# Kernel optimization log

Measured on AMD Instinct MI355X. Metric: run time of the kernel, lower is better.

The kernel has to match this reference:

```python
import jax, jax.numpy as jnp
import numpy as np

N = 100000      # nodes
E = 3200000     # edges
F = 128         # input features
H = 16          # hiddenSize (hard-coded in source)
C = 10          # num_classes
RATIO = 0.25
K1 = int(np.ceil(RATIO * N))   # 25000 nodes kept by pool1
K2 = int(np.ceil(RATIO * K1))  # 6250 nodes kept by pool2


def gcn_conv(x, W, b, src, dst, ew, n):
    """PyG GCNConv: add self-loops (weight 1), symmetric normalization.
    ew carries edge validity mask / weights; ew=0 edges are exactly equivalent
    to removed edges (contribute nothing to degree or aggregation)."""
    h = x @ W                                                   # [n, out]
    deg = jax.ops.segment_sum(ew, dst, num_segments=n) + 1.0    # +1 self-loop
    dinv = jax.lax.rsqrt(deg)
    norm = dinv[src] * dinv[dst] * ew                           # [E]
    agg = jax.ops.segment_sum(h[src] * norm[:, None], dst, num_segments=n)
    agg = agg + h * (dinv * dinv)[:, None]                      # self-loop msg
    return agg + b


def graph_conv_score(x, wroot, wrel, b, src, dst, ew, n):
    """PyG GraphConv (SAGPooling default GNN) with out_channels=1:
    score_i = x_i @ Wroot + (sum_j x_j) @ Wrel + b."""
    agg = jax.ops.segment_sum(x[src] * ew[:, None], dst, num_segments=n)
    return (x @ wroot + agg @ wrel + b).reshape(-1)             # [n]


def sag_pool(x, src, dst, ew, wroot, wrel, b, n, k):
    """SAGPooling: score -> top-k -> x[perm]*tanh(score[perm]) -> filter_adj.
    filter_adj is expressed by relabeling kept nodes and zeroing dropped edges
    (math-identical to edge removal for downstream GCN/GraphConv)."""
    score = graph_conv_score(x, wroot, wrel, b, src, dst, ew, n)
    vals, perm = jax.lax.top_k(score, k)
    xp = x[perm] * jnp.tanh(vals)[:, None]
    new_idx = jnp.full((n,), -1, dtype=jnp.int32).at[perm].set(
        jnp.arange(k, dtype=jnp.int32))
    ns, nd = new_idx[src], new_idx[dst]
    valid = (ns >= 0) & (nd >= 0)
    new_ew = jnp.where(valid, ew, 0.0)
    ns = jnp.where(valid, ns, 0)
    nd = jnp.where(valid, nd, 0)
    return xp, ns, nd, new_ew


def setup_inputs() -> dict:
    key = jax.random.key(0)
    ks = jax.random.split(key, 9)
    s = 0.1
    return {
        "x": jax.random.normal(ks[0], (N, F), jnp.float32),
        "edge_src": jax.random.randint(ks[1], (E,), 0, N, dtype=jnp.int32),
        "edge_dst": jax.random.randint(ks[2], (E,), 0, N, dtype=jnp.int32),
        "W1": jax.random.normal(ks[3], (F, H), jnp.float32) * s,
        "b1": jnp.zeros((H,), jnp.float32),
        "p1_wroot": jax.random.normal(ks[4], (H, 1), jnp.float32) * s,
        "p1_wrel": jax.random.normal(ks[5], (H, 1), jnp.float32) * s,
        "p1_b": jnp.zeros((1,), jnp.float32),
        "W2": jax.random.normal(ks[6], (H, C), jnp.float32) * s,
        "b2": jnp.zeros((C,), jnp.float32),
        "p2_wroot": jax.random.normal(ks[7], (C, 1), jnp.float32) * s,
        "p2_wrel": jax.random.normal(ks[8], (C, 1), jnp.float32) * s,
        "p2_b": jnp.zeros((1,), jnp.float32),
    }


def reference(x, edge_src, edge_dst, W1, b1, p1_wroot, p1_wrel, p1_b,
              W2, b2, p2_wroot, p2_wrel, p2_b):
    ew0 = jnp.ones((E,), x.dtype)
    # conv1 + relu (dropout is identity in eval mode)
    h = jax.nn.relu(gcn_conv(x, W1, b1, edge_src, edge_dst, ew0, N))
    # pool1 (ratio 0.25)
    x1, s1, d1, ew1 = sag_pool(h, edge_src, edge_dst, ew0,
                               p1_wroot, p1_wrel, p1_b, N, K1)
    # conv2
    h2 = gcn_conv(x1, W2, b2, s1, d1, ew1, K1)
    # pool2 (ratio 0.25)
    x2, s2, d2, ew2 = sag_pool(h2, s1, d1, ew1,
                               p2_wroot, p2_wrel, p2_b, K1, K2)
    # global mean pool over the single graph, then log_softmax
    out = jnp.mean(x2, axis=0, keepdims=True)   # [1, C]
    return jax.nn.log_softmax(out, axis=1)
```

## Files before the change

### kernel.cpp

```cpp
#include <hip/hip_runtime.h>
#include <math.h>

#define NN 100000
#define EE 3200000
#define FF 128
#define HH 16
#define CC 10
#define PC 12
#define KK1 25000
#define KK2 6250

#define NBIN 512
#define BUCK_SHIFT 8
#define BUCK_MASK 255
#define ABLK 256
#define EPB (EE / ABLK)
#define NBUCK ((NN + 255) / 256)

struct SelState {
  unsigned prefix;
  unsigned kcur;
  unsigned ctr_gt;
  unsigned ctr_eq;
  unsigned hist[256];
};

__device__ __forceinline__ unsigned fkey(float f) {
  unsigned u = __float_as_uint(f);
  return (u & 0x80000000u) ? ~u : (u | 0x80000000u);
}

__global__ __launch_bounds__(256) void k_xw1(const float* __restrict__ x,
                                             const float* __restrict__ W1,
                                             float* __restrict__ h0) {
  __shared__ float sW[FF * HH];
  __shared__ float sx[16][FF];
  int t = threadIdx.x;
  for (int i = t; i < FF * HH; i += 256) sW[i] = W1[i];
  int base = blockIdx.x * 16;
  for (int i = t; i < 16 * FF; i += 256) {
    int r = i >> 7, c = i & 127;
    int node = base + r;
    sx[r][c] = (node < NN) ? x[(size_t)node * FF + c] : 0.f;
  }
  __syncthreads();
  int r = t >> 4;
  int o = t & 15;
  float acc = 0.f;
#pragma unroll
  for (int k = 0; k < FF; ++k) acc += sx[r][k] * sW[k * HH + o];
  int node = base + r;
  if (node < NN) h0[node * HH + o] = acc;
}

__global__ __launch_bounds__(256) void k_bhist(const int* __restrict__ dst,
                                               unsigned* __restrict__ Hist) {
  __shared__ unsigned sh[NBIN];
  int t = threadIdx.x;
  for (int i = t; i < NBIN; i += 256) sh[i] = 0;
  __syncthreads();
  int base = blockIdx.x * EPB;
  for (int i = base + t; i < base + EPB; i += 256)
    atomicAdd(&sh[dst[i] >> BUCK_SHIFT], 1u);
  __syncthreads();
  for (int i = t; i < NBIN; i += 256) Hist[blockIdx.x * NBIN + i] = sh[i];
}

__global__ __launch_bounds__(64) void k_bcursor(unsigned* __restrict__ Hist,
                                                unsigned* __restrict__ Tot) {
  int bin = blockIdx.x * 64 + threadIdx.x;
  unsigned run = 0;
#pragma unroll 8
  for (int b = 0; b < ABLK; ++b) {
    unsigned c = Hist[b * NBIN + bin];
    Hist[b * NBIN + bin] = run;
    run += c;
  }
  Tot[bin] = run;
}

__global__ __launch_bounds__(512) void k_bscan(const unsigned* __restrict__ Tot,
                                               unsigned* __restrict__ BucketOff) {
  __shared__ unsigned s[NBIN];
  int t = threadIdx.x;
  unsigned v = Tot[t];
  s[t] = v;
  __syncthreads();
  for (int off = 1; off < NBIN; off <<= 1) {
    unsigned u = (t >= off) ? s[t - off] : 0;
    __syncthreads();
    s[t] += u;
    __syncthreads();
  }
  BucketOff[t] = s[t] - v;
  if (t == NBIN - 1) BucketOff[NBIN] = s[t];
}

__global__ __launch_bounds__(256) void k_bscatter(const int* __restrict__ src,
                                                  const int* __restrict__ dst,
                                                  const unsigned* __restrict__ Hist,
                                                  const unsigned* __restrict__ BucketOff,
                                                  unsigned* __restrict__ packed) {
  __shared__ unsigned cur[NBIN];
  int t = threadIdx.x;
  for (int i = t; i < NBIN; i += 256)
    cur[i] = BucketOff[i] + Hist[blockIdx.x * NBIN + i];
  __syncthreads();
  int base = blockIdx.x * EPB;
  for (int i = base + t; i < base + EPB; i += 256) {
    int d = dst[i];
    unsigned pos = atomicAdd(&cur[d >> BUCK_SHIFT], 1u);
    packed[pos] = ((unsigned)(d & BUCK_MASK) << 17) | (unsigned)src[i];
  }
}

__global__ __launch_bounds__(256) void k_bfine(const unsigned* __restrict__ packed,
                                               const unsigned* __restrict__ BucketOff,
                                               int* __restrict__ rowstart,
                                               float* __restrict__ dinv,
                                               int* __restrict__ csr) {
  __shared__ unsigned fcnt[256], fpos[256], fcur[256];
  int bin = blockIdx.x;
  int t = threadIdx.x;
  unsigned b0 = BucketOff[bin], b1 = BucketOff[bin + 1];
  fcnt[t] = 0;
  __syncthreads();
  for (unsigned e = b0 + t; e < b1; e += 256)
    atomicAdd(&fcnt[packed[e] >> 17], 1u);
  __syncthreads();
  unsigned v = fcnt[t];
  fpos[t] = v;
  __syncthreads();
  for (int off = 1; off < 256; off <<= 1) {
    unsigned u = (t >= off) ? fpos[t - off] : 0;
    __syncthreads();
    fpos[t] += u;
    __syncthreads();
  }
  unsigned excl = fpos[t] - v;
  fcur[t] = b0 + excl;
  int node = bin * 256 + t;
  if (node < NN) {
    rowstart[node] = (int)(b0 + excl);
    dinv[node] = rsqrtf((float)v + 1.0f);
  }
  if (bin == 0 && t == 0) rowstart[NN] = EE;
  __syncthreads();
  for (unsigned e = b0 + t; e < b1; e += 256) {
    unsigned p = packed[e];
    unsigned pos = atomicAdd(&fcur[p >> 17], 1u);
    csr[pos] = (int)(p & 0x1FFFFu);
  }
}

__global__ __launch_bounds__(256) void k_conv1(const float* __restrict__ h0,
                                               const float* __restrict__ dinv,
                                               const int* __restrict__ rowstart,
                                               const int* __restrict__ csr,
                                               const float* __restrict__ b1,
                                               const float* __restrict__ wroot,
                                               const float* __restrict__ wrel,
                                               const float* __restrict__ bp,
                                               float* __restrict__ h,
                                               float* __restrict__ score,
                                               float* __restrict__ hrel) {
  int node = blockIdx.x * 4 + (threadIdx.x >> 6);
  if (node >= NN) return;
  int lane = threadIdx.x & 63;
  int eslot = lane >> 2;
  int kq = lane & 3;
  int s0 = rowstart[node], s1 = rowstart[node + 1];
  float ax = 0.f, ay = 0.f, az = 0.f, aw = 0.f;
  for (int base = s0; base < s1; base += 16) {
    int idx = base + eslot;
    bool on = idx < s1;
    int sv = on ? csr[idx] : 0;
    float dv = on ? dinv[sv] : 0.f;
    float4 hv = *(const float4*)(h0 + sv * HH + kq * 4);
    ax += hv.x * dv;
    ay += hv.y * dv;
    az += hv.z * dv;
    aw += hv.w * dv;
  }
#pragma unroll
  for (int m = 4; m <= 32; m <<= 1) {
    ax += __shfl_xor(ax, m);
    ay += __shfl_xor(ay, m);
    az += __shfl_xor(az, m);
    aw += __shfl_xor(aw, m);
  }
  float di = dinv[node];
  float4 hs = *(const float4*)(h0 + node * HH + kq * 4);
  float vx = ax * di + hs.x * di * di + b1[kq * 4 + 0];
  float vy = ay * di + hs.y * di * di + b1[kq * 4 + 1];
  float vz = az * di + hs.z * di * di + b1[kq * 4 + 2];
  float vw = aw * di + hs.w * di * di + b1[kq * 4 + 3];
  vx = vx > 0.f ? vx : 0.f;
  vy = vy > 0.f ? vy : 0.f;
  vz = vz > 0.f ? vz : 0.f;
  vw = vw > 0.f ? vw : 0.f;
  if (eslot == 0) {
    float4 o4 = make_float4(vx, vy, vz, vw);
    *(float4*)(h + node * HH + kq * 4) = o4;
  }
  float sr = vx * wroot[kq * 4] + vy * wroot[kq * 4 + 1] +
             vz * wroot[kq * 4 + 2] + vw * wroot[kq * 4 + 3];
  float sl = vx * wrel[kq * 4] + vy * wrel[kq * 4 + 1] +
             vz * wrel[kq * 4 + 2] + vw * wrel[kq * 4 + 3];
  sr += __shfl_xor(sr, 1);
  sr += __shfl_xor(sr, 2);
  sl += __shfl_xor(sl, 1);
  sl += __shfl_xor(sl, 2);
  if (lane == 0) {
    score[node] = sr + bp[0];
    hrel[node] = sl;
  }
}

__global__ __launch_bounds__(256) void k_scoreg(const int* __restrict__ rowstart,
                                                const int* __restrict__ csr,
                                                const float* __restrict__ hrel,
                                                float* __restrict__ score) {
  int node = blockIdx.x * 16 + (threadIdx.x >> 4);
  if (node >= NN) return;
  int lane = threadIdx.x & 15;
  int s0 = rowstart[node], s1 = rowstart[node + 1];
  float sum = 0.f;
  for (int e = s0 + lane; e < s1; e += 16) sum += hrel[csr[e]];
#pragma unroll
  for (int m = 8; m; m >>= 1) sum += __shfl_xor(sum, m, 16);
  if (lane == 0) score[node] += sum;
}

__global__ void k_state_init(SelState* st, int K) {
  if (threadIdx.x == 0) {
    st->prefix = 0;
    st->kcur = (unsigned)K;
    st->ctr_gt = 0;
    st->ctr_eq = 0;
  }
  st->hist[threadIdx.x] = 0;
}

__global__ __launch_bounds__(256) void k_hist(const float* __restrict__ vals, int n,
                                              SelState* st, int pass) {
  __shared__ unsigned sh[256];
  int t = threadIdx.x;
  sh[t] = 0;
  __syncthreads();
  int i = blockIdx.x * 256 + t;
  if (i < n) {
    unsigned key = fkey(vals[i]);
    bool ok = true;
    if (pass != 0) ok = (key >> (32 - 8 * pass)) == st->prefix;
    if (ok) atomicAdd(&sh[(key >> (24 - 8 * pass)) & 255], 1u);
  }
  __syncthreads();
  if (sh[t]) atomicAdd(&st->hist[t], sh[t]);
}

__global__ __launch_bounds__(256) void k_scan(SelState* st) {
  __shared__ unsigned s[256];
  int t = threadIdx.x;
  unsigned kcur = st->kcur;
  unsigned v = st->hist[t];
  s[t] = v;
  __syncthreads();
  for (int off = 1; off < 256; off <<= 1) {
    unsigned u = (t + off < 256) ? s[t + off] : 0;
    __syncthreads();
    s[t] += u;
    __syncthreads();
  }
  unsigned Sme = s[t];
  unsigned Snext = (t < 255) ? s[t + 1] : 0;
  if (Sme >= kcur && Snext < kcur) {
    st->prefix = (st->prefix << 8) | (unsigned)t;
    st->kcur = kcur - Snext;
  }
  st->hist[t] = 0;
}

__global__ void k_select1(const float* __restrict__ score, const float* __restrict__ h,
                          SelState* st, int* __restrict__ new_idx,
                          int* __restrict__ orig_of, float* __restrict__ x1) {
  int i = blockIdx.x * blockDim.x + threadIdx.x;
  if (i >= NN) return;
  float sc = score[i];
  unsigned key = fkey(sc);
  unsigned T = st->prefix;
  int id = -1;
  if (key > T) {
    id = (int)atomicAdd(&st->ctr_gt, 1u);
  } else if (key == T) {
    unsigned p = atomicAdd(&st->ctr_eq, 1u);
    unsigned kneed = st->kcur;
    if (p < kneed) id = (KK1 - (int)kneed) + (int)p;
  }
  new_idx[i] = id;
  if (id >= 0) {
    orig_of[id] = i;
    float tv = tanhf(sc);
#pragma unroll
    for (int k = 0; k < HH; ++k) x1[id * HH + k] = h[i * HH + k] * tv;
  }
}

__global__ __launch_bounds__(256) void k_deg2(const int* __restrict__ orig_of,
                                              const int* __restrict__ rowstart,
                                              const int* __restrict__ csr,
                                              const int* __restrict__ nidx,
                                              float* __restrict__ dinv2) {
  int j = blockIdx.x * 16 + (threadIdx.x >> 4);
  if (j >= KK1) return;
  int lane = threadIdx.x & 15;
  int o = orig_of[j];
  int s0 = rowstart[o], s1 = rowstart[o + 1];
  int c = 0;
  for (int e = s0 + lane; e < s1; e += 16) c += (nidx[csr[e]] >= 0) ? 1 : 0;
#pragma unroll
  for (int m = 8; m; m >>= 1) c += __shfl_xor(c, m, 16);
  if (lane == 0) dinv2[j] = rsqrtf((float)c + 1.0f);
}

__global__ void k_xw2(const float* __restrict__ x1, const float* __restrict__ W2,
                      float* __restrict__ h20) {
  int t = blockIdx.x * blockDim.x + threadIdx.x;
  if (t >= KK1 * PC) return;
  int node = t / PC;
  int o = t - node * PC;
  float acc = 0.f;
  if (o < CC) {
#pragma unroll
    for (int k = 0; k < HH; ++k) acc += x1[node * HH + k] * W2[k * CC + o];
  }
  h20[t] = acc;
}

__global__ __launch_bounds__(256) void k_conv2(const float* __restrict__ h20,
                                               const float* __restrict__ dinv2,
                                               const int* __restrict__ orig_of,
                                               const int* __restrict__ rowstart,
                                               const int* __restrict__ csr,
                                               const int* __restrict__ nidx,
                                               const float* __restrict__ b2,
                                               const float* __restrict__ wroot,
                                               const float* __restrict__ wrel,
                                               const float* __restrict__ bp,
                                               float* __restrict__ h2,
                                               float* __restrict__ score2,
                                               float* __restrict__ h2rel) {
  int j = blockIdx.x * 4 + (threadIdx.x >> 6);
  if (j >= KK1) return;
  int lane = threadIdx.x & 63;
  int eslot = lane >> 2;
  int kq = lane & 3;
  int o = orig_of[j];
  int s0 = rowstart[o], s1 = rowstart[o + 1];
  float ax = 0.f, ay = 0.f, az = 0.f, aw = 0.f;
  for (int base = s0; base < s1; base += 16) {
    int idx = base + eslot;
    bool on = idx < s1;
    int sv = on ? nidx[csr[idx]] : -1;
    float dv = (sv >= 0) ? dinv2[sv] : 0.f;
    int sva = (sv >= 0) ? sv : 0;
    float4 hv = *(const float4*)(h20 + sva * PC + ((kq < 3) ? kq * 4 : 8));
    if (kq == 3) dv = 0.f;
    ax += hv.x * dv;
    ay += hv.y * dv;
    az += hv.z * dv;
    aw += hv.w * dv;
  }
#pragma unroll
  for (int m = 4; m <= 32; m <<= 1) {
    ax += __shfl_xor(ax, m);
    ay += __shfl_xor(ay, m);
    az += __shfl_xor(az, m);
    aw += __shfl_xor(aw, m);
  }
  float di = dinv2[j];
  int kb = (kq < 3) ? kq * 4 : 8;
  float4 hs = *(const float4*)(h20 + j * PC + kb);
  float bx = (kb + 0 < CC) ? b2[kb + 0] : 0.f;
  float by = (kb + 1 < CC) ? b2[kb + 1] : 0.f;
  float bz = (kb + 2 < CC) ? b2[kb + 2] : 0.f;
  float bw = (kb + 3 < CC) ? b2[kb + 3] : 0.f;
  float vx = ax * di + hs.x * di * di + bx;
  float vy = ay * di + hs.y * di * di + by;
  float vz = az * di + hs.z * di * di + bz;
  float vw = aw * di + hs.w * di * di + bw;
  if (kq == 3) { vx = vy = vz = vw = 0.f; }
  if (kb + 2 >= CC) vz = 0.f;
  if (kb + 3 >= CC) vw = 0.f;
  if (eslot == 0 && kq < 3) {
    float4 o4 = make_float4(vx, vy, vz, vw);
    *(float4*)(h2 + j * PC + kq * 4) = o4;
  }
  float wrx = (kb + 0 < CC) ? wroot[kb + 0] : 0.f;
  float wry = (kb + 1 < CC) ? wroot[kb + 1] : 0.f;
  float wrz = (kb + 2 < CC) ? wroot[kb + 2] : 0.f;
  float wrw = (kb + 3 < CC) ? wroot[kb + 3] : 0.f;
  float wlx = (kb + 0 < CC) ? wrel[kb + 0] : 0.f;
  float wly = (kb + 1 < CC) ? wrel[kb + 1] : 0.f;
  float wlz = (kb + 2 < CC) ? wrel[kb + 2] : 0.f;
  float wlw = (kb + 3 < CC) ? wrel[kb + 3] : 0.f;
  float sr = (kq == 3) ? 0.f : (vx * wrx + vy * wry + vz * wrz + vw * wrw);
  float sl = (kq == 3) ? 0.f : (vx * wlx + vy * wly + vz * wlz + vw * wlw);
  sr += __shfl_xor(sr, 1);
  sr += __shfl_xor(sr, 2);
  sl += __shfl_xor(sl, 1);
  sl += __shfl_xor(sl, 2);
  if (lane == 0) {
    score2[j] = sr + bp[0];
    h2rel[j] = sl;
  }
}

__global__ __launch_bounds__(256) void k_score2g(const int* __restrict__ orig_of,
                                                 const int* __restrict__ rowstart,
                                                 const int* __restrict__ csr,
                                                 const int* __restrict__ nidx,
                                                 const float* __restrict__ h2rel,
                                                 float* __restrict__ score2) {
  int j = blockIdx.x * 16 + (threadIdx.x >> 4);
  if (j >= KK1) return;
  int lane = threadIdx.x & 15;
  int o = orig_of[j];
  int s0 = rowstart[o], s1 = rowstart[o + 1];
  float sum = 0.f;
  for (int e = s0 + lane; e < s1; e += 16) {
    int s = nidx[csr[e]];
    if (s >= 0) sum += h2rel[s];
  }
#pragma unroll
  for (int m = 8; m; m >>= 1) sum += __shfl_xor(sum, m, 16);
  if (lane == 0) score2[j] += sum;
}

__global__ __launch_bounds__(256) void k_final_accum(const float* __restrict__ score,
                                                     const float* __restrict__ h2,
                                                     SelState* st, float* __restrict__ acc) {
  int i = blockIdx.x * blockDim.x + threadIdx.x;
  float tv = 0.f;
  if (i < KK1) {
    float sc = score[i];
    unsigned key = fkey(sc);
    unsigned T = st->prefix;
    bool keep = false;
    if (key > T) {
      keep = true;
    } else if (key == T) {
      unsigned p = atomicAdd(&st->ctr_eq, 1u);
      keep = (p < st->kcur);
    }
    if (keep) tv = tanhf(sc);
  }
  __shared__ float sacc[CC];
  if (threadIdx.x < CC) sacc[threadIdx.x] = 0.f;
  __syncthreads();
#pragma unroll
  for (int c = 0; c < CC; ++c) {
    float v = (i < KK1 && tv != 0.f) ? h2[i * PC + c] * tv : 0.f;
#pragma unroll
    for (int m = 32; m; m >>= 1) v += __shfl_xor(v, m, 64);
    if ((threadIdx.x & 63) == 0) atomicAdd(&sacc[c], v);
  }
  __syncthreads();
  if (threadIdx.x < CC) atomicAdd(&acc[threadIdx.x], sacc[threadIdx.x]);
}

__global__ void k_final(const float* __restrict__ acc, float* __restrict__ out) {
  if (threadIdx.x != 0 || blockIdx.x != 0) return;
  float v[CC];
  float m = -1e30f;
#pragma unroll
  for (int c = 0; c < CC; ++c) {
    v[c] = acc[c] / (float)KK2;
    if (v[c] > m) m = v[c];
  }
  float s = 0.f;
#pragma unroll
  for (int c = 0; c < CC; ++c) s += expf(v[c] - m);
  float l = logf(s);
#pragma unroll
  for (int c = 0; c < CC; ++c) out[c] = v[c] - m - l;
}

extern "C" void kernel_launch(void* const* d_in, const int* in_sizes, int n_in,
                              void* d_out, int out_size, void* d_ws, size_t ws_size,
                              hipStream_t stream) {
  const float* x      = (const float*)d_in[0];
  const int*   esrc   = (const int*)d_in[1];
  const int*   edst   = (const int*)d_in[2];
  const float* W1     = (const float*)d_in[3];
  const float* b1     = (const float*)d_in[4];
  const float* w1root = (const float*)d_in[5];
  const float* w1rel  = (const float*)d_in[6];
  const float* p1b    = (const float*)d_in[7];
  const float* W2     = (const float*)d_in[8];
  const float* b2     = (const float*)d_in[9];
  const float* w2root = (const float*)d_in[10];
  const float* w2rel  = (const float*)d_in[11];
  const float* p2b    = (const float*)d_in[12];
  float* out = (float*)d_out;

  char* w = (char*)d_ws;
  size_t off = 0;
  auto alloc = [&](size_t bytes) -> char* {
    char* p = w + off;
    off += (bytes + 255) & ~(size_t)255;
    return p;
  };
  float*    h0      = (float*)alloc((size_t)NN * HH * 4);
  float*    hbuf    = (float*)alloc((size_t)NN * HH * 4);
  float*    dinv1   = (float*)alloc((size_t)NN * 4);
  float*    hrel1   = (float*)alloc((size_t)NN * 4);
  float*    score1  = (float*)alloc((size_t)NN * 4);
  int*      nidx    = (int*)  alloc((size_t)NN * 4);
  int*      csr     = (int*)  alloc((size_t)EE * 4);
  unsigned* packed  = (unsigned*)alloc((size_t)EE * 4);
  int*      rowst   = (int*)  alloc((size_t)(NN + 1) * 4);
  unsigned* Hist    = (unsigned*)alloc((size_t)ABLK * NBIN * 4);
  unsigned* Tot     = (unsigned*)alloc((size_t)NBIN * 4);
  unsigned* BOff    = (unsigned*)alloc((size_t)(NBIN + 1) * 4);
  SelState* st1     = (SelState*)alloc(sizeof(SelState));
  SelState* st2     = (SelState*)alloc(sizeof(SelState));
  float*    acc     = (float*)alloc(256);

  size_t off2 = 0;
  auto alloc2 = [&](size_t bytes) -> char* {
    char* p = (char*)h0 + off2;
    off2 += (bytes + 255) & ~(size_t)255;
    return p;
  };
  float* x1      = (float*)alloc2((size_t)KK1 * HH * 4);
  float* h20     = (float*)alloc2((size_t)KK1 * PC * 4 + 256);
  float* h2      = (float*)alloc2((size_t)KK1 * PC * 4 + 256);
  float* dinv2   = (float*)alloc2((size_t)KK1 * 4);
  float* h2rel   = (float*)alloc2((size_t)KK1 * 4);
  float* score2  = (float*)alloc2((size_t)KK1 * 4);
  int*   orig_of = (int*)  alloc2((size_t)KK1 * 4);

  const int BN  = (NN + 255) / 256;
  const int BK1 = (KK1 + 255) / 256;

  k_xw1<<<NN / 16, 256, 0, stream>>>(x, W1, h0);

  k_bhist<<<ABLK, 256, 0, stream>>>(edst, Hist);
  k_bcursor<<<NBIN / 64, 64, 0, stream>>>(Hist, Tot);
  k_bscan<<<1, NBIN, 0, stream>>>(Tot, BOff);
  k_bscatter<<<ABLK, 256, 0, stream>>>(esrc, edst, Hist, BOff, packed);
  k_bfine<<<NBUCK, 256, 0, stream>>>(packed, BOff, rowst, dinv1, csr);

  k_conv1<<<(NN + 3) / 4, 256, 0, stream>>>(h0, dinv1, rowst, csr, b1, w1root, w1rel,
                                            p1b, hbuf, score1, hrel1);
  k_scoreg<<<(NN + 15) / 16, 256, 0, stream>>>(rowst, csr, hrel1, score1);

  k_state_init<<<1, 256, 0, stream>>>(st1, KK1);
  for (int p = 0; p < 4; ++p) {
    k_hist<<<BN, 256, 0, stream>>>(score1, NN, st1, p);
    k_scan<<<1, 256, 0, stream>>>(st1);
  }
  k_select1<<<BN, 256, 0, stream>>>(score1, hbuf, st1, nidx, orig_of, x1);

  k_deg2<<<(KK1 + 15) / 16, 256, 0, stream>>>(orig_of, rowst, csr, nidx, dinv2);
  k_xw2<<<(KK1 * PC + 255) / 256, 256, 0, stream>>>(x1, W2, h20);
  k_conv2<<<(KK1 + 3) / 4, 256, 0, stream>>>(h20, dinv2, orig_of, rowst, csr, nidx,
                                             b2, w2root, w2rel, p2b, h2, score2, h2rel);
  k_score2g<<<(KK1 + 15) / 16, 256, 0, stream>>>(orig_of, rowst, csr, nidx, h2rel, score2);

  k_state_init<<<1, 256, 0, stream>>>(st2, KK2);
  for (int p = 0; p < 4; ++p) {
    k_hist<<<BK1, 256, 0, stream>>>(score2, KK1, st2, p);
    k_scan<<<1, 256, 0, stream>>>(st2);
  }
  hipMemsetAsync(acc, 0, CC * 4, stream);
  k_final_accum<<<BK1, 256, 0, stream>>>(score2, h2, st2, acc);
  k_final<<<1, 64, 0, stream>>>(acc, out);
}
```

Baseline: 477.9 us.

## Merge small kernels, unroll conv1 gather, and use ballot-based compaction in select

Several independent kernels are merged into combined launches: the two state inits and the acc memset become one kernel, xw1 and the bucket histogram share a grid, bcursor and bscan become one block, and deg2 and xw2 share a grid. The conv1 edge loop is unrolled four ways with separate accumulators to expose more memory-level parallelism. The select kernel replaces per-thread global atomics with wave ballots and one atomic per block. The goal is fewer launches and less atomic contention. The single-block bcursor_scan serializes 256 row reads per thread, which may be slower than the old 8-block version.

```diff
diff --git a/kernel.cpp b/kernel.cpp
--- a/kernel.cpp
+++ b/kernel.cpp
@@ -16,6 +16,10 @@
 #define ABLK 256
 #define EPB (EE / ABLK)
 #define NBUCK ((NN + 255) / 256)
+#define XW1_BLKS (NN / 16)
+
+#define DEG2_BLKS ((KK1 + 15) / 16)
+#define XW2_BLKS ((KK1 * PC + 255) / 256)
 
 struct SelState {
   unsigned prefix;
@@ -30,60 +34,66 @@
   return (u & 0x80000000u) ? ~u : (u | 0x80000000u);
 }
 
-__global__ __launch_bounds__(256) void k_xw1(const float* __restrict__ x,
-                                             const float* __restrict__ W1,
-                                             float* __restrict__ h0) {
-  __shared__ float sW[FF * HH];
-  __shared__ float sx[16][FF];
+__global__ __launch_bounds__(512) void k_state_combo(SelState* st1, SelState* st2,
+                                                     float* acc) {
   int t = threadIdx.x;
-  for (int i = t; i < FF * HH; i += 256) sW[i] = W1[i];
-  int base = blockIdx.x * 16;
-  for (int i = t; i < 16 * FF; i += 256) {
-    int r = i >> 7, c = i & 127;
-    int node = base + r;
-    sx[r][c] = (node < NN) ? x[(size_t)node * FF + c] : 0.f;
-  }
-  __syncthreads();
-  int r = t >> 4;
-  int o = t & 15;
-  float acc = 0.f;
-#pragma unroll
-  for (int k = 0; k < FF; ++k) acc += sx[r][k] * sW[k * HH + o];
-  int node = base + r;
-  if (node < NN) h0[node * HH + o] = acc;
-}
-
-__global__ __launch_bounds__(256) void k_bhist(const int* __restrict__ dst,
-                                               unsigned* __restrict__ Hist) {
-  __shared__ unsigned sh[NBIN];
+  unsigned* a1 = (unsigned*)st1;
+  unsigned* a2 = (unsigned*)st2;
+  const int W = sizeof(SelState) / 4;
+  if (t < W) a1[t] = 0u;
+  if (t < W) a2[t] = 0u;
+  if (t < CC) acc[t] = 0.f;
+  if (t == 0) { st1->kcur = KK1; st2->kcur = KK2; }
+}
+
+__global__ __launch_bounds__(256) void k_xw1_bhist(const float* __restrict__ x,
+                                                   const float* __restrict__ W1,
+                                                   float* __restrict__ h0,
+                                                   const int* __restrict__ dst,
+                                                   unsigned* __restrict__ Hist) {
+  __shared__ float smem[FF * HH + 16 * FF];
+  int b = blockIdx.x;
   int t = threadIdx.x;
-  for (int i = t; i < NBIN; i += 256) sh[i] = 0;
-  __syncthreads();
-  int base = blockIdx.x * EPB;
-  for (int i = base + t; i < base + EPB; i += 256)
-    atomicAdd(&sh[dst[i] >> BUCK_SHIFT], 1u);
-  __syncthreads();
-  for (int i = t; i < NBIN; i += 256) Hist[blockIdx.x * NBIN + i] = sh[i];
-}
-
-__global__ __launch_bounds__(64) void k_bcursor(unsigned* __restrict__ Hist,
-                                                unsigned* __restrict__ Tot) {
-  int bin = blockIdx.x * 64 + threadIdx.x;
-  unsigned run = 0;
-#pragma unroll 8
-  for (int b = 0; b < ABLK; ++b) {
-    unsigned c = Hist[b * NBIN + bin];
-    Hist[b * NBIN + bin] = run;
-    run += c;
-  }
-  Tot[bin] = run;
-}
-
-__global__ __launch_bounds__(512) void k_bscan(const unsigned* __restrict__ Tot,
-                                               unsigned* __restrict__ BucketOff) {
+  if (b < XW1_BLKS) {
+    float* sW = smem;
+    float* sx = smem + FF * HH;
+    for (int i = t; i < FF * HH; i += 256) sW[i] = W1[i];
+    int base = b * 16;
+    for (int i = t; i < 16 * FF; i += 256) {
+      int r = i >> 7, c = i & 127;
+      sx[r * FF + c] = x[(size_t)(base + r) * FF + c];
+    }
+    __syncthreads();
+    int r = t >> 4;
+    int o = t & 15;
+    float acc = 0.f;
+#pragma unroll
+    for (int k = 0; k < FF; ++k) acc += sx[r * FF + k] * sW[k * HH + o];
+    h0[(base + r) * HH + o] = acc;
+  } else {
+    unsigned* sh = (unsigned*)smem;
+    int blk = b - XW1_BLKS;
+    for (int i = t; i < NBIN; i += 256) sh[i] = 0;
+    __syncthreads();
+    int base = blk * EPB;
+    for (int i = base + t; i < base + EPB; i += 256)
+      atomicAdd(&sh[dst[i] >> BUCK_SHIFT], 1u);
+    __syncthreads();
+    for (int i = t; i < NBIN; i += 256) Hist[blk * NBIN + i] = sh[i];
+  }
+}
+
+__global__ __launch_bounds__(512) void k_bcursor_scan(unsigned* __restrict__ Hist,
+                                                      unsigned* __restrict__ BucketOff) {
   __shared__ unsigned s[NBIN];
   int t = threadIdx.x;
-  unsigned v = Tot[t];
+  unsigned run = 0;
+  for (int b = 0; b < ABLK; ++b) {
+    unsigned c = Hist[b * NBIN + t];
+    Hist[b * NBIN + t] = run;
+    run += c;
+  }
+  unsigned v = run;
   s[t] = v;
   __syncthreads();
   for (int off = 1; off < NBIN; off <<= 1) {
@@ -170,18 +180,35 @@
   int eslot = lane >> 2;
   int kq = lane & 3;
   int s0 = rowstart[node], s1 = rowstart[node + 1];
-  float ax = 0.f, ay = 0.f, az = 0.f, aw = 0.f;
-  for (int base = s0; base < s1; base += 16) {
-    int idx = base + eslot;
-    bool on = idx < s1;
-    int sv = on ? csr[idx] : 0;
-    float dv = on ? dinv[sv] : 0.f;
-    float4 hv = *(const float4*)(h0 + sv * HH + kq * 4);
-    ax += hv.x * dv;
-    ay += hv.y * dv;
-    az += hv.z * dv;
-    aw += hv.w * dv;
-  }
+  float4 a0 = make_float4(0.f, 0.f, 0.f, 0.f);
+  float4 a1 = a0, a2 = a0, a3 = a0;
+  for (int base = s0; base < s1; base += 64) {
+    int i0 = base + eslot;
+    int i1 = base + 16 + eslot;
+    int i2 = base + 32 + eslot;
+    int i3 = base + 48 + eslot;
+    bool o0 = i0 < s1, o1 = i1 < s1, o2 = i2 < s1, o3 = i3 < s1;
+    int v0 = o0 ? csr[i0] : 0;
+    int v1 = o1 ? csr[i1] : 0;
+    int v2 = o2 ? csr[i2] : 0;
+    int v3 = o3 ? csr[i3] : 0;
+    float d0 = o0 ? dinv[v0] : 0.f;
+    float d1 = o1 ? dinv[v1] : 0.f;
+    float d2 = o2 ? dinv[v2] : 0.f;
+    float d3 = o3 ? dinv[v3] : 0.f;
+    float4 h0v = *(const float4*)(h0 + v0 * HH + kq * 4);
+    float4 h1v = *(const float4*)(h0 + v1 * HH + kq * 4);
+    float4 h2v = *(const float4*)(h0 + v2 * HH + kq * 4);
+    float4 h3v = *(const float4*)(h0 + v3 * HH + kq * 4);
+    a0.x += h0v.x * d0; a0.y += h0v.y * d0; a0.z += h0v.z * d0; a0.w += h0v.w * d0;
+    a1.x += h1v.x * d1; a1.y += h1v.y * d1; a1.z += h1v.z * d1; a1.w += h1v.w * d1;
+    a2.x += h2v.x * d2; a2.y += h2v.y * d2; a2.z += h2v.z * d2; a2.w += h2v.w * d2;
+    a3.x += h3v.x * d3; a3.y += h3v.y * d3; a3.z += h3v.z * d3; a3.w += h3v.w * d3;
+  }
+  float ax = (a0.x + a1.x) + (a2.x + a3.x);
+  float ay = (a0.y + a1.y) + (a2.y + a3.y);
+  float az = (a0.z + a1.z) + (a2.z + a3.z);
+  float aw = (a0.w + a1.w) + (a2.w + a3.w);
 #pragma unroll
   for (int m = 4; m <= 32; m <<= 1) {
     ax += __shfl_xor(ax, m);
@@ -232,16 +259,6 @@
   if (lane == 0) score[node] += sum;
 }
 
-__global__ void k_state_init(SelState* st, int K) {
-  if (threadIdx.x == 0) {
-    st->prefix = 0;
-    st->kcur = (unsigned)K;
-    st->ctr_gt = 0;
-    st->ctr_eq = 0;
-  }
-  st->hist[threadIdx.x] = 0;
-}
-
 __global__ __launch_bounds__(256) void k_hist(const float* __restrict__ vals, int n,
                                               SelState* st, int pass) {
   __shared__ unsigned sh[256];
@@ -281,19 +298,49 @@
   st->hist[t] = 0;
 }
 
-__global__ void k_select1(const float* __restrict__ score, const float* __restrict__ h,
-                          SelState* st, int* __restrict__ new_idx,
-                          int* __restrict__ orig_of, float* __restrict__ x1) {
-  int i = blockIdx.x * blockDim.x + threadIdx.x;
+__global__ __launch_bounds__(256) void k_select1(const float* __restrict__ score,
+                                                 const float* __restrict__ h,
+                                                 SelState* st, int* __restrict__ new_idx,
+                                                 int* __restrict__ orig_of,
+                                                 float* __restrict__ x1) {
+  int i = blockIdx.x * 256 + threadIdx.x;
+  int lane = threadIdx.x & 63;
+  int wid = threadIdx.x >> 6;
+  float sc = 0.f;
+  bool gt = false, eq = false;
+  unsigned T = st->prefix;
+  if (i < NN) {
+    sc = score[i];
+    unsigned key = fkey(sc);
+    gt = key > T;
+    eq = key == T;
+  }
+  unsigned long long mgt = __ballot(gt);
+  unsigned long long meq = __ballot(eq);
+  __shared__ int wgt[4], weq[4];
+  if (lane == 0) {
+    wgt[wid] = __popcll(mgt);
+    weq[wid] = __popcll(meq);
+  }
+  __syncthreads();
+  if (threadIdx.x == 0) {
+    int tg = wgt[0] + wgt[1] + wgt[2] + wgt[3];
+    int te = weq[0] + weq[1] + weq[2] + weq[3];
+    int bg = tg ? (int)atomicAdd(&st->ctr_gt, (unsigned)tg) : 0;
+    int be = te ? (int)atomicAdd(&st->ctr_eq, (unsigned)te) : 0;
+    int r = bg;
+    for (int w2 = 0; w2 < 4; ++w2) { int c = wgt[w2]; wgt[w2] = r; r += c; }
+    r = be;
+    for (int w2 = 0; w2 < 4; ++w2) { int c = weq[w2]; weq[w2] = r; r += c; }
+  }
+  __syncthreads();
   if (i >= NN) return;
-  float sc = score[i];
-  unsigned key = fkey(sc);
-  unsigned T = st->prefix;
+  unsigned long long ltmask = (1ull << lane) - 1ull;
   int id = -1;
-  if (key > T) {
-    id = (int)atomicAdd(&st->ctr_gt, 1u);
-  } else if (key == T) {
-    unsigned p = atomicAdd(&st->ctr_eq, 1u);
+  if (gt) {
+    id = wgt[wid] + (int)__popcll(mgt & ltmask);
+  } else if (eq) {
+    unsigned p = (unsigned)(weq[wid] + (int)__popcll(meq & ltmask));
     unsigned kneed = st->kcur;
     if (p < kneed) id = (KK1 - (int)kneed) + (int)p;
   }
@@ -306,35 +353,38 @@
   }
 }
 
-__global__ __launch_bounds__(256) void k_deg2(const int* __restrict__ orig_of,
-                                              const int* __restrict__ rowstart,
-                                              const int* __restrict__ csr,
-                                              const int* __restrict__ nidx,
-                                              float* __restrict__ dinv2) {
-  int j = blockIdx.x * 16 + (threadIdx.x >> 4);
-  if (j >= KK1) return;
-  int lane = threadIdx.x & 15;
-  int o = orig_of[j];
-  int s0 = rowstart[o], s1 = rowstart[o + 1];
-  int c = 0;
-  for (int e = s0 + lane; e < s1; e += 16) c += (nidx[csr[e]] >= 0) ? 1 : 0;
-#pragma unroll
-  for (int m = 8; m; m >>= 1) c += __shfl_xor(c, m, 16);
-  if (lane == 0) dinv2[j] = rsqrtf((float)c + 1.0f);
-}
-
-__global__ void k_xw2(const float* __restrict__ x1, const float* __restrict__ W2,
-                      float* __restrict__ h20) {
-  int t = blockIdx.x * blockDim.x + threadIdx.x;
-  if (t >= KK1 * PC) return;
-  int node = t / PC;
-  int o = t - node * PC;
-  float acc = 0.f;
-  if (o < CC) {
-#pragma unroll
-    for (int k = 0; k < HH; ++k) acc += x1[node * HH + k] * W2[k * CC + o];
-  }
-  h20[t] = acc;
+__global__ __launch_bounds__(256) void k_deg2xw2(const int* __restrict__ orig_of,
+                                                 const int* __restrict__ rowstart,
+                                                 const int* __restrict__ csr,
+                                                 const int* __restrict__ nidx,
+                                                 float* __restrict__ dinv2,
+                                                 const float* __restrict__ x1,
+                                                 const float* __restrict__ W2,
+                                                 float* __restrict__ h20) {
+  int b = blockIdx.x;
+  if (b < DEG2_BLKS) {
+    int j = b * 16 + (threadIdx.x >> 4);
+    if (j >= KK1) return;
+    int lane = threadIdx.x & 15;
+    int o = orig_of[j];
+    int s0 = rowstart[o], s1 = rowstart[o + 1];
+    int c = 0;
+    for (int e = s0 + lane; e < s1; e += 16) c += (nidx[csr[e]] >= 0) ? 1 : 0;
+#pragma unroll
+    for (int m = 8; m; m >>= 1) c += __shfl_xor(c, m, 16);
+    if (lane == 0) dinv2[j] = rsqrtf((float)c + 1.0f);
+  } else {
+    int t = (b - DEG2_BLKS) * 256 + threadIdx.x;
+    if (t >= KK1 * PC) return;
+    int node = t / PC;
+    int o = t - node * PC;
+    float acc = 0.f;
+    if (o < CC) {
+#pragma unroll
+      for (int k = 0; k < HH; ++k) acc += x1[node * HH + k] * W2[k * CC + o];
+    }
+    h20[t] = acc;
+  }
 }
 
 __global__ __launch_bounds__(256) void k_conv2(const float* __restrict__ h20,
@@ -521,7 +571,6 @@
   unsigned* packed  = (unsigned*)alloc((size_t)EE * 4);
   int*      rowst   = (int*)  alloc((size_t)(NN + 1) * 4);
   unsigned* Hist    = (unsigned*)alloc((size_t)ABLK * NBIN * 4);
-  unsigned* Tot     = (unsigned*)alloc((size_t)NBIN * 4);
   unsigned* BOff    = (unsigned*)alloc((size_t)(NBIN + 1) * 4);
   SelState* st1     = (SelState*)alloc(sizeof(SelState));
   SelState* st2     = (SelState*)alloc(sizeof(SelState));
@@ -544,11 +593,11 @@
   const int BN  = (NN + 255) / 256;
   const int BK1 = (KK1 + 255) / 256;
 
-  k_xw1<<<NN / 16, 256, 0, stream>>>(x, W1, h0);
-
-  k_bhist<<<ABLK, 256, 0, stream>>>(edst, Hist);
-  k_bcursor<<<NBIN / 64, 64, 0, stream>>>(Hist, Tot);
-  k_bscan<<<1, NBIN, 0, stream>>>(Tot, BOff);
+  k_state_combo<<<1, 512, 0, stream>>>(st1, st2, acc);
+
+  k_xw1_bhist<<<XW1_BLKS + ABLK, 256, 0, stream>>>(x, W1, h0, edst, Hist);
+
+  k_bcursor_scan<<<1, 512, 0, stream>>>(Hist, BOff);
   k_bscatter<<<ABLK, 256, 0, stream>>>(esrc, edst, Hist, BOff, packed);
   k_bfine<<<NBUCK, 256, 0, stream>>>(packed, BOff, rowst, dinv1, csr);
 
@@ -556,25 +605,22 @@
                                             p1b, hbuf, score1, hrel1);
   k_scoreg<<<(NN + 15) / 16, 256, 0, stream>>>(rowst, csr, hrel1, score1);
 
-  k_state_init<<<1, 256, 0, stream>>>(st1, KK1);
   for (int p = 0; p < 4; ++p) {
     k_hist<<<BN, 256, 0, stream>>>(score1, NN, st1, p);
     k_scan<<<1, 256, 0, stream>>>(st1);
   }
   k_select1<<<BN, 256, 0, stream>>>(score1, hbuf, st1, nidx, orig_of, x1);
 
-  k_deg2<<<(KK1 + 15) / 16, 256, 0, stream>>>(orig_of, rowst, csr, nidx, dinv2);
-  k_xw2<<<(KK1 * PC + 255) / 256, 256, 0, stream>>>(x1, W2, h20);
+  k_deg2xw2<<<DEG2_BLKS + XW2_BLKS, 256, 0, stream>>>(orig_of, rowst, csr, nidx,
+                                                      dinv2, x1, W2, h20);
   k_conv2<<<(KK1 + 3) / 4, 256, 0, stream>>>(h20, dinv2, orig_of, rowst, csr, nidx,
                                              b2, w2root, w2rel, p2b, h2, score2, h2rel);
   k_score2g<<<(KK1 + 15) / 16, 256, 0, stream>>>(orig_of, rowst, csr, nidx, h2rel, score2);
 
-  k_state_init<<<1, 256, 0, stream>>>(st2, KK2);
   for (int p = 0; p < 4; ++p) {
     k_hist<<<BK1, 256, 0, stream>>>(score2, KK1, st2, p);
     k_scan<<<1, 256, 0, stream>>>(st2);
   }
-  hipMemsetAsync(acc, 0, CC * 4, stream);
   k_final_accum<<<BK1, 256, 0, stream>>>(score2, h2, st2, acc);
   k_final<<<1, 64, 0, stream>>>(acc, out);
 }
```

After: 429.2 us. 10.2% less time.
